# Optimization experiments

Hardware: AMD Instinct MI355X
Metric: run time of the kernel (lower is better)

The kernel has to match this reference:

```python
import jax, jax.numpy as jnp
import numpy as np

D = 512
H_MAX = 32
W_MAX = 32
BATCH = 16


def _embeds_1d(L: int, d: int) -> jnp.ndarray:
    # Faithful to torch _embeds_1d: denom = L ** (2*cumsum(ones)/d) = L**(2*(j+1)/d)
    # (numer broadcast interpreted as per-position arange over rows, the intended math)
    numer = jnp.arange(L, dtype=jnp.float32)[:, None]            # [L,1]
    exps = 2.0 * jnp.arange(1, d + 1, dtype=jnp.float32) / d     # [d]
    denom = jnp.float32(L) ** exps                               # [d]
    e = numer / denom                                            # [L,d]
    return jnp.zeros_like(e).at[:, 0::2].set(jnp.sin(e[:, 0::2])).at[:, 1::2].set(jnp.cos(e[:, 1::2]))


def make_embed(H: int, W: int, d: int) -> jnp.ndarray:
    # [H,W,d] = embed_h[:,None,:] + embed_w[None,:,:]
    return _embeds_1d(H, d)[:, None, :] + _embeds_1d(W, d)[None, :, :]


def setup_inputs() -> dict:
    key = jax.random.key(0)
    k1, k2 = jax.random.split(key)
    q = jax.random.normal(k1, (BATCH, H_MAX, W_MAX, D), dtype=jnp.float32)
    k = jax.random.normal(k2, (BATCH, H_MAX, W_MAX, D), dtype=jnp.float32)
    embed = make_embed(H_MAX, W_MAX, D)
    return {"q": q, "k": k, "embed": embed}


def reference(q, k, embed):
    # content->position logits + position->(content+position) logits
    # q: [b,i,j,d], k: [b,k,l,d], embed: [i,j,d] (= q_embed = k_embed)
    logits = (jnp.einsum('bijd,kld->bijkl', q, embed)
              + jnp.einsum('ijd,bkld->bijkl', embed, k + embed))
    return logits  # [b,i,j,k,l]
```

## Files before the change

kernel.cpp:

```cpp
#include <hip/hip_runtime.h>
#include <stdint.h>

#define DD 512
#define NP 1024
#define NB 16

typedef __attribute__((ext_vector_type(8))) __bf16 bf16x8;
typedef __attribute__((ext_vector_type(4))) float f32x4;


__device__ __forceinline__ bf16x8 cvt8(const float4& a, const float4& b) {
    bf16x8 r;
    r[0]=(__bf16)a.x; r[1]=(__bf16)a.y; r[2]=(__bf16)a.z; r[3]=(__bf16)a.w;
    r[4]=(__bf16)b.x; r[5]=(__bf16)b.y; r[6]=(__bf16)b.z; r[7]=(__bf16)b.w;
    return r;
}

__device__ __forceinline__ void gload_lds16(const void* g, void* l) {
    __builtin_amdgcn_global_load_lds(
        (const __attribute__((address_space(1))) unsigned int*)g,
        (__attribute__((address_space(3))) unsigned int*)l,
        16, 0, 0);
}

__device__ __forceinline__ bf16x8 ehw_row(const float* __restrict__ embed, int r,
                                          int col, const float4& z0, const float4& z1) {
    int srcrow = (r < 32) ? (r << 5) : (r - 32);
    const float* sp = embed + (size_t)srcrow * DD + col;
    float4 a = *(const float4*)sp;
    float4 b = *(const float4*)(sp + 4);
    if (r >= 32) {
        a.x -= z0.x; a.y -= z0.y; a.z -= z0.z; a.w -= z0.w;
        b.x -= z1.x; b.y -= z1.y; b.z -= z1.z; b.w -= z1.w;
    }
    return cvt8(a, b);
}

__global__ __launch_bounds__(256) void prep(
    const float* __restrict__ embed, unsigned short* __restrict__ tbl,
    float* __restrict__ G)
{
    const int tid = threadIdx.x;
    if (blockIdx.x < 16) {
        int g = blockIdx.x * 256 + tid;
        int row = g >> 6;
        int c8  = (g & 63) * 8;
        float4 z0 = *(const float4*)(embed + c8);
        float4 z1 = *(const float4*)(embed + c8 + 4);
        bf16x8 r = ehw_row(embed, row, c8, z0, z1);
        int h  = c8 >> 8;
        int cl = c8 & 255;
        int byte = (cl * 2) ^ ((row & 7) << 4);
        *(bf16x8*)((char*)tbl + h * 32768 + row * 512 + byte) = r;
    } else {
        const int lane = tid & 63, wid = tid >> 6;
        const int lr = lane & 15, kq = (lane >> 4) * 8;
        f32x4 acc[4];
        #pragma unroll
        for (int n = 0; n < 4; ++n) acc[n] = (f32x4)0.0f;
        for (int ks = 0; ks < 16; ++ks) {
            int col = ks * 32 + kq;
            float4 z0 = *(const float4*)(embed + col);
            float4 z1 = *(const float4*)(embed + col + 4);
            bf16x8 af = ehw_row(embed, wid * 16 + lr, col, z0, z1);
            #pragma unroll
            for (int n = 0; n < 4; ++n) {
                bf16x8 bf = ehw_row(embed, n * 16 + lr, col, z0, z1);
                acc[n] = __builtin_amdgcn_mfma_f32_16x16x32_bf16(af, bf, acc[n], 0, 0, 0);
            }
        }
        int row0 = wid * 16 + (lane >> 4) * 4;
        #pragma unroll
        for (int n = 0; n < 4; ++n)
            #pragma unroll
            for (int i = 0; i < 4; ++i)
                G[(size_t)(row0 + i) * 64 + n * 16 + lr] = acc[n][i];
    }
}

__global__ __launch_bounds__(256) void rank_gemm(
    const float* __restrict__ q, const float* __restrict__ kin,
    const unsigned short* __restrict__ tbl,
    float* __restrict__ qhw, float* __restrict__ khw)
{
    __shared__ __align__(16) unsigned short T[64 * 512];

    const int tid = threadIdx.x, lane = tid & 63, wid = tid >> 6;
    const int lr = lane & 15, kq = (lane >> 4) * 8;
    const int gsel = blockIdx.x >> 8;
    const int tile = blockIdx.x & 255;

    #pragma unroll
    for (int c = 0; c < 16; ++c) {
        int off = wid * 16384 + c * 1024;
        gload_lds16((const char*)tbl + off + lane * 16, (char*)T + off);
    }

    const int grow = tile * 64 + wid * 16 + lr;
    const float* srcA = (gsel ? kin : q) + (size_t)grow * DD + kq;

    f32x4 acc[4];
    #pragma unroll
    for (int n = 0; n < 4; ++n) acc[n] = (f32x4)0.0f;
    __syncthreads();

    #pragma unroll 8
    for (int ks = 0; ks < 16; ++ks) {
        float4 a0 = *(const float4*)(srcA + ks * 32);
        float4 a1 = *(const float4*)(srcA + ks * 32 + 4);
        bf16x8 sf = cvt8(a0, a1);
        const char* Th = (const char*)T + (ks >> 3) * 32768;
        int kb = ((ks & 7) * 32 + kq) * 2;
        bf16x8 ef[4];
        #pragma unroll
        for (int n = 0; n < 4; ++n) {
            int row = n * 16 + lr;
            ef[n] = *(const bf16x8*)(Th + row * 512 + (kb ^ ((row & 7) << 4)));
        }
        if (!gsel) {
            #pragma unroll
            for (int n = 0; n < 4; ++n)
                acc[n] = __builtin_amdgcn_mfma_f32_16x16x32_bf16(sf, ef[n], acc[n], 0, 0, 0);
        } else {
            #pragma unroll
            for (int n = 0; n < 4; ++n)
                acc[n] = __builtin_amdgcn_mfma_f32_16x16x32_bf16(ef[n], sf, acc[n], 0, 0, 0);
        }
    }

    if (!gsel) {
        float* o = qhw + (size_t)(tile * 64 + wid * 16 + (lane >> 4) * 4) * 64 + lr;
        #pragma unroll
        for (int n = 0; n < 4; ++n)
            #pragma unroll
            for (int i = 0; i < 4; ++i)
                o[(size_t)i * 64 + n * 16] = acc[n][i];
    } else {
        int b = grow >> 10, Q = grow & 1023;
        float* o = khw + (size_t)b * 65536 + Q;
        int m0 = (lane >> 4) * 4;
        #pragma unroll
        for (int n = 0; n < 4; ++n)
            #pragma unroll
            for (int i = 0; i < 4; ++i)
                o[(size_t)(n * 16 + m0 + i) * 1024] = acc[n][i];
    }
}

__global__ __launch_bounds__(256) void assemble(
    const float* __restrict__ qhw, const float* __restrict__ khw,
    const float* __restrict__ G, float* __restrict__ out)
{
    __shared__ __align__(16) float kh[NP];
    __shared__ __align__(16) float d1[16][32];
    __shared__ __align__(16) float d2[16][32];

    const int tid = threadIdx.x, wid = tid >> 6, lane = tid & 63;
    const int b  = blockIdx.x >> 6;
    const int i  = (blockIdx.x >> 1) & 31;
    const int jh = blockIdx.x & 1;

    gload_lds16((const char*)(khw + (size_t)b * 65536 + (size_t)i * 1024)
                    + wid * 1024 + lane * 16,
                (char*)kh + wid * 1024);

    {
        int jj = tid >> 4, c = tid & 15;
        int j  = jh * 16 + jj;
        size_t Prow = (size_t)b * NP + i * 32 + j;
        const float* qA = qhw + Prow * 64;
        const float* Gi = G + (size_t)i * 64;
        const float* Gj = G + (size_t)(32 + j) * 64;
        d1[jj][c]      = qA[c]      + Gi[c]      + Gj[c];
        d1[jj][c + 16] = qA[c + 16] + Gi[c + 16] + Gj[c + 16];
        d2[jj][c]      = qA[32 + c] + Gi[32 + c] + Gj[32 + c];
        d2[jj][c + 16] = qA[48 + c] + Gi[48 + c] + Gj[48 + c];
    }
    __syncthreads();

    const int Q0 = tid * 4;
    const int kidx = Q0 >> 5;
    const int lidx = Q0 & 31;
    const float4 khv = *(const float4*)&kh[Q0];

    float* orow = out + ((size_t)b * NP + i * 32 + jh * 16) * NP + Q0;
    const float* kwb = khw + (size_t)b * 65536 + (size_t)(32 + jh * 16) * 1024 + Q0;

    #pragma unroll 4
    for (int jj = 0; jj < 16; ++jj) {
        float4 kw = *(const float4*)(kwb + (size_t)jj * 1024);
        float  s1 = d1[jj][kidx];
        float4 s2 = *(const float4*)&d2[jj][lidx];
        f32x4 v;
        v.x = khv.x + kw.x + s1 + s2.x;
        v.y = khv.y + kw.y + s1 + s2.y;
        v.z = khv.z + kw.z + s1 + s2.z;
        v.w = khv.w + kw.w + s1 + s2.w;
        __builtin_nontemporal_store(v, (f32x4*)(orow + (size_t)jj * NP));
    }
}

extern "C" void kernel_launch(void* const* d_in, const int* in_sizes, int n_in,
                              void* d_out, int out_size, void* d_ws, size_t ws_size,
                              hipStream_t stream) {
    const float* q = (const float*)d_in[0];
    const float* k = (const float*)d_in[1];
    const float* e = (const float*)d_in[2];
    float* out = (float*)d_out;

    float* qhw = (float*)d_ws;
    float* khw = qhw + (size_t)NB * NP * 64;
    unsigned short* tbl = (unsigned short*)(khw + (size_t)NB * 64 * NP);
    float* G = (float*)((char*)tbl + 65536);

    hipLaunchKernelGGL(prep,      dim3(17),   dim3(256), 0, stream, e, tbl, G);
    hipLaunchKernelGGL(rank_gemm, dim3(512),  dim3(256), 0, stream, q, k, tbl, qhw, khw);
    hipLaunchKernelGGL(assemble,  dim3(1024), dim3(256), 0, stream, qhw, khw, G, out);
}
```

Measured before the change: 52.81 us.

## Retile rank_gemm to 32-row tiles with halved LDS table staging

```diff
diff --git a/kernel.cpp b/kernel.cpp
--- a/kernel.cpp
+++ b/kernel.cpp
@@ -83,67 +83,71 @@
     const unsigned short* __restrict__ tbl,
     float* __restrict__ qhw, float* __restrict__ khw)
 {
-    __shared__ __align__(16) unsigned short T[64 * 512];
+    __shared__ __align__(16) unsigned short T[64 * 256];
 
     const int tid = threadIdx.x, lane = tid & 63, wid = tid >> 6;
     const int lr = lane & 15, kq = (lane >> 4) * 8;
-    const int gsel = blockIdx.x >> 8;
-    const int tile = blockIdx.x & 255;
+    const int gsel = blockIdx.x >> 9;
+    const int tile = blockIdx.x & 511;
+    const int tw = wid * 16;
+
+    const int grow = tile * 32;
+    const float* s0 = (gsel ? kin : q) + (size_t)(grow + lr) * DD + kq;
+
+    f32x4 acc0 = (f32x4)0.0f, acc1 = (f32x4)0.0f;
 
     #pragma unroll
-    for (int c = 0; c < 16; ++c) {
-        int off = wid * 16384 + c * 1024;
-        gload_lds16((const char*)tbl + off + lane * 16, (char*)T + off);
-    }
-
-    const int grow = tile * 64 + wid * 16 + lr;
-    const float* srcA = (gsel ? kin : q) + (size_t)grow * DD + kq;
-
-    f32x4 acc[4];
-    #pragma unroll
-    for (int n = 0; n < 4; ++n) acc[n] = (f32x4)0.0f;
-    __syncthreads();
-
-    #pragma unroll 8
-    for (int ks = 0; ks < 16; ++ks) {
-        float4 a0 = *(const float4*)(srcA + ks * 32);
-        float4 a1 = *(const float4*)(srcA + ks * 32 + 4);
-        bf16x8 sf = cvt8(a0, a1);
-        const char* Th = (const char*)T + (ks >> 3) * 32768;
-        int kb = ((ks & 7) * 32 + kq) * 2;
-        bf16x8 ef[4];
-        #pragma unroll
-        for (int n = 0; n < 4; ++n) {
-            int row = n * 16 + lr;
-            ef[n] = *(const bf16x8*)(Th + row * 512 + (kb ^ ((row & 7) << 4)));
-        }
-        if (!gsel) {
-            #pragma unroll
-            for (int n = 0; n < 4; ++n)
-                acc[n] = __builtin_amdgcn_mfma_f32_16x16x32_bf16(sf, ef[n], acc[n], 0, 0, 0);
-        } else {
-            #pragma unroll
-            for (int n = 0; n < 4; ++n)
-                acc[n] = __builtin_amdgcn_mfma_f32_16x16x32_bf16(ef[n], sf, acc[n], 0, 0, 0);
+    for (int half = 0; half < 2; ++half) {
+        if (half) {
+            asm volatile("s_waitcnt lgkmcnt(0)" ::: "memory");
+            __builtin_amdgcn_sched_barrier(0);
+        }
+        #pragma unroll
+        for (int c = 0; c < 8; ++c) {
+            int off = tw * 512 + c * 1024;
+            gload_lds16((const char*)tbl + half * 32768 + off + lane * 16,
+                        (char*)T + off);
+        }
+        asm volatile("s_waitcnt vmcnt(0)" ::: "memory");
+        __builtin_amdgcn_sched_barrier(0);
+
+        #pragma unroll
+        for (int ks = 0; ks < 8; ++ks) {
+            const float* sa = s0 + half * 256 + ks * 32;
+            float4 a0 = *(const float4*)sa;
+            float4 a1 = *(const float4*)(sa + 4);
+            float4 b0 = *(const float4*)(sa + 16 * DD);
+            float4 b1 = *(const float4*)(sa + 16 * DD + 4);
+            bf16x8 sf0 = cvt8(a0, a1);
+            bf16x8 sf1 = cvt8(b0, b1);
+            const int row = tw + lr;
+            const int kb = (ks * 32 + kq) * 2;
+            bf16x8 ef = *(const bf16x8*)((const char*)T + row * 512 +
+                                         (kb ^ ((row & 7) << 4)));
+            if (!gsel) {
+                acc0 = __builtin_amdgcn_mfma_f32_16x16x32_bf16(sf0, ef, acc0, 0, 0, 0);
+                acc1 = __builtin_amdgcn_mfma_f32_16x16x32_bf16(sf1, ef, acc1, 0, 0, 0);
+            } else {
+                acc0 = __builtin_amdgcn_mfma_f32_16x16x32_bf16(ef, sf0, acc0, 0, 0, 0);
+                acc1 = __builtin_amdgcn_mfma_f32_16x16x32_bf16(ef, sf1, acc1, 0, 0, 0);
+            }
         }
     }
 
     if (!gsel) {
-        float* o = qhw + (size_t)(tile * 64 + wid * 16 + (lane >> 4) * 4) * 64 + lr;
-        #pragma unroll
-        for (int n = 0; n < 4; ++n)
-            #pragma unroll
-            for (int i = 0; i < 4; ++i)
-                o[(size_t)i * 64 + n * 16] = acc[n][i];
+        float* o = qhw + (size_t)(grow + (lane >> 4) * 4) * 64 + tw + lr;
+        #pragma unroll
+        for (int i = 0; i < 4; ++i) o[(size_t)i * 64]          = acc0[i];
+        #pragma unroll
+        for (int i = 0; i < 4; ++i) o[(size_t)(16 + i) * 64]   = acc1[i];
     } else {
-        int b = grow >> 10, Q = grow & 1023;
-        float* o = khw + (size_t)b * 65536 + Q;
-        int m0 = (lane >> 4) * 4;
-        #pragma unroll
-        for (int n = 0; n < 4; ++n)
-            #pragma unroll
-            for (int i = 0; i < 4; ++i)
-                o[(size_t)(n * 16 + m0 + i) * 1024] = acc[n][i];
+        int b = grow >> 10, Q0 = grow & 1023;
+        float* o = khw + (size_t)b * 65536
+                 + (size_t)(tw + (lane >> 4) * 4) * 1024 + Q0 + lr;
+        #pragma unroll
+        for (int i = 0; i < 4; ++i) o[(size_t)i * 1024]        = acc0[i];
+        #pragma unroll
+        for (int i = 0; i < 4; ++i) o[(size_t)i * 1024 + 16]   = acc1[i];
     }
 }
 
@@ -214,6 +218,6 @@
     float* G = (float*)((char*)tbl + 65536);
 
     hipLaunchKernelGGL(prep,      dim3(17),   dim3(256), 0, stream, e, tbl, G);
-    hipLaunchKernelGGL(rank_gemm, dim3(512),  dim3(256), 0, stream, q, k, tbl, qhw, khw);
+    hipLaunchKernelGGL(rank_gemm, dim3(1024), dim3(256), 0, stream, q, k, tbl, qhw, khw);
     hipLaunchKernelGGL(assemble,  dim3(1024), dim3(256), 0, stream, qhw, khw, G, out);
 }
```

Result: slower. 72.15 us (+36.6%).
